# Kernel optimization log

Measured on AMD Instinct MI355X. Metric: run time of the kernel, lower is better.

Reference implementation:

```python
import jax, jax.numpy as jnp
import numpy as np

B, S, H, NH = 4, 2048, 2048, 16
HD = H // NH
EPS = 1e-5


def setup_inputs() -> dict:
    key = jax.random.key(0)
    ks = jax.random.split(key, 5)
    return {
        "x": jax.random.normal(ks[0], (B, S, H), dtype=jnp.float32),
        "ln_w": jnp.ones((H,), dtype=jnp.float32),
        "ln_b": jnp.zeros((H,), dtype=jnp.float32),
        "c_attn_w": jax.random.normal(ks[1], (H, 3 * H), dtype=jnp.float32) * 0.02,
        "c_attn_b": jax.random.normal(ks[2], (3 * H,), dtype=jnp.float32) * 0.02,
        "c_proj_w": jax.random.normal(ks[3], (H, H), dtype=jnp.float32) * 0.02,
        "c_proj_b": jax.random.normal(ks[4], (H,), dtype=jnp.float32) * 0.02,
    }


def reference(x, ln_w, ln_b, c_attn_w, c_attn_b, c_proj_w, c_proj_b):
    residual = x
    # fused layer norm
    mu = jnp.mean(x, axis=-1, keepdims=True)
    var = jnp.mean(jnp.square(x - mu), axis=-1, keepdims=True)
    xn = (x - mu) * jax.lax.rsqrt(var + EPS) * ln_w + ln_b
    qkv = jnp.einsum("bsh,hk->bsk", xn, c_attn_w) + c_attn_b
    q, k, v = jnp.split(qkv, 3, axis=-1)
    def heads(t):
        return t.reshape(B, S, NH, HD).transpose(0, 2, 1, 3)
    q, k, v = heads(q), heads(k), heads(v)
    # causal flash attention (reference math)
    scale = 1.0 / np.sqrt(HD)
    scores = jnp.einsum("bnqd,bnkd->bnqk", q, k) * scale
    causal = jnp.tril(jnp.ones((S, S), dtype=bool))
    scores = jnp.where(causal, scores, jnp.finfo(scores.dtype).min)
    attn = jax.nn.softmax(scores, axis=-1)
    o = jnp.einsum("bnqk,bnkd->bnqd", attn, v)
    # merge heads: [B,NH,S,HD] -> [B,S,H]
    o = o.transpose(0, 2, 1, 3).reshape(B, S, H)
    # output projection + residual (fused_ffn, add_gelu=False, dropout=0)
    return jnp.einsum("bsh,hk->bsk", o, c_proj_w) + c_proj_b + residual
```

## Files before the change

kernel.cpp:

```cpp
#include <hip/hip_runtime.h>
#include <stdint.h>
#include <math.h>

#define B_  4
#define S_  2048
#define H_  2048
#define NH_ 16
#define HD_ 128
#define M_  (B_*S_)
#define N3_ (3*H_)
#define NQT_ (S_/64)
#define NT_ (H_/64)

typedef __attribute__((ext_vector_type(8))) short short8;
typedef __attribute__((ext_vector_type(4))) float floatx4;
typedef unsigned int u32;

__device__ __forceinline__ unsigned short f2bf(float f) {
  unsigned u = __float_as_uint(f);
  u += 0x7FFF + ((u >> 16) & 1);
  return (unsigned short)(u >> 16);
}

__device__ __forceinline__ void gl2lds16(const void* g, void* l) {
  __builtin_amdgcn_global_load_lds(
      (const __attribute__((address_space(1))) u32*)g,
      (__attribute__((address_space(3))) u32*)l, 16, 0, 0);
}

__global__ __launch_bounds__(256) void ln_kernel(
    const float* __restrict__ x, const float* __restrict__ w,
    const float* __restrict__ b, unsigned short* __restrict__ xn) {
  int row = blockIdx.x;
  int t = threadIdx.x;
  const float* xr = x + (size_t)row * H_;
  float4 v0 = *(const float4*)(xr + t * 4);
  float4 v1 = *(const float4*)(xr + 1024 + t * 4);
  float s  = v0.x + v0.y + v0.z + v0.w + v1.x + v1.y + v1.z + v1.w;
  float sq = v0.x*v0.x + v0.y*v0.y + v0.z*v0.z + v0.w*v0.w
           + v1.x*v1.x + v1.y*v1.y + v1.z*v1.z + v1.w*v1.w;
  #pragma unroll
  for (int m = 32; m; m >>= 1) { s += __shfl_xor(s, m); sq += __shfl_xor(sq, m); }
  __shared__ float red[8];
  int wv = t >> 6;
  if ((t & 63) == 0) { red[wv * 2] = s; red[wv * 2 + 1] = sq; }
  __syncthreads();
  s  = red[0] + red[2] + red[4] + red[6];
  sq = red[1] + red[3] + red[5] + red[7];
  float mu  = s * (1.0f / H_);
  float var = sq * (1.0f / H_) - mu * mu;
  float rs  = rsqrtf(var + 1e-5f);

  float4 w0 = *(const float4*)(w + t * 4);
  float4 b0 = *(const float4*)(b + t * 4);
  float4 w1 = *(const float4*)(w + 1024 + t * 4);
  float4 b1 = *(const float4*)(b + 1024 + t * 4);
  ushort4 o0, o1;
  o0.x = f2bf((v0.x - mu) * rs * w0.x + b0.x);
  o0.y = f2bf((v0.y - mu) * rs * w0.y + b0.y);
  o0.z = f2bf((v0.z - mu) * rs * w0.z + b0.z);
  o0.w = f2bf((v0.w - mu) * rs * w0.w + b0.w);
  o1.x = f2bf((v1.x - mu) * rs * w1.x + b1.x);
  o1.y = f2bf((v1.y - mu) * rs * w1.y + b1.y);
  o1.z = f2bf((v1.z - mu) * rs * w1.z + b1.z);
  o1.w = f2bf((v1.w - mu) * rs * w1.w + b1.w);
  unsigned short* orow = xn + (size_t)row * H_;
  *(ushort4*)(orow + t * 4) = o0;
  *(ushort4*)(orow + 1024 + t * 4) = o1;
}

__global__ __launch_bounds__(256) void transpose_f2b(
    const float* __restrict__ in, unsigned short* __restrict__ out,
    int R, int C) {
  __shared__ float tile[32][33];
  int tx = threadIdx.x & 31, ty = threadIdx.x >> 5;
  int c0 = blockIdx.x * 32, r0 = blockIdx.y * 32;
  #pragma unroll
  for (int i = 0; i < 32; i += 8)
    tile[ty + i][tx] = in[(size_t)(r0 + ty + i) * C + c0 + tx];
  __syncthreads();
  #pragma unroll
  for (int i = 0; i < 32; i += 8)
    out[(size_t)(c0 + ty + i) * R + r0 + tx] = f2bf(tile[tx][ty + i]);
}

__device__ __forceinline__ void gemm256_acc(
    const unsigned short* __restrict__ A, const unsigned short* __restrict__ Bt,
    int m0, int n0, unsigned short (*sh)[16384], floatx4 (&acc)[8][4]) {
  const int t = threadIdx.x;
  const int lane = t & 63, wv = t >> 6;
  const int l15 = lane & 15, quad = lane >> 4;
  const int wm = wv >> 2, wn = wv & 3;
  const int x7 = l15 & 7;

  const int aRB = (wm * 128 + l15) * 64;
  const int bRB = (wn * 64 + l15) * 64;
  const int kx0 = ((0 + quad) ^ x7) * 8;
  const int kx1 = ((4 + quad) ^ x7) * 8;

  const int r = t >> 3, cc = t & 7;
  const int scol = (cc ^ (r & 7)) * 8;
  const unsigned short* aSrc = A + (size_t)(m0 + r) * H_ + scol;
  const int btr = (r >> 5) * 64 + (r & 31);
  const unsigned short* bSrc = Bt + (size_t)(n0 + btr) * H_ + scol;
  const int aDst = t * 8;
  const int bDst = (r >> 5) * 4096 + (r & 31) * 64 + cc * 8;

  auto stageA = [&](int kt, int reg, int buf) {
    const unsigned short* s = aSrc + (size_t)(reg * 64) * H_ + kt * 64;
    unsigned short* d = sh[buf * 2] + aDst + reg * 4096;
    gl2lds16(s, d);
    gl2lds16(s + (size_t)128 * H_, d + 8192);
  };
  auto stageB = [&](int kt, int reg, int buf) {
    const unsigned short* s = bSrc + (size_t)(reg * 32) * H_ + kt * 64;
    unsigned short* d = sh[buf * 2 + 1] + bDst + reg * 2048;
    gl2lds16(s, d);
    gl2lds16(s + (size_t)128 * H_, d + 8192);
  };

  #pragma unroll
  for (int i = 0; i < 8; i++)
    #pragma unroll
    for (int j = 0; j < 4; j++) acc[i][j] = (floatx4){0.f, 0.f, 0.f, 0.f};

  stageA(0, 0, 0); stageB(0, 0, 0); stageA(0, 1, 0); stageB(0, 1, 0);
  stageA(1, 0, 1); stageB(1, 0, 1); stageA(1, 1, 1);
  asm volatile("s_waitcnt vmcnt(6)" ::: "memory");
  __builtin_amdgcn_s_barrier();

  short8 aR[4][2], b01[2][2], b23[2][2];

  for (int n = 0; n < NT_; ++n) {
    const int buf = n & 1;
    const unsigned short* Ab = sh[buf * 2];
    const unsigned short* Bb = sh[buf * 2 + 1];

    #pragma unroll
    for (int i = 0; i < 4; ++i) {
      aR[i][0] = *(const short8*)(Ab + aRB + i * 1024 + kx0);
      aR[i][1] = *(const short8*)(Ab + aRB + i * 1024 + kx1);
    }
    #pragma unroll
    for (int j = 0; j < 2; ++j) {
      b01[j][0] = *(const short8*)(Bb + bRB + j * 1024 + kx0);
      b01[j][1] = *(const short8*)(Bb + bRB + j * 1024 + kx1);
    }
    if (n + 1 < NT_) stageB(n + 1, 1, buf ^ 1);
    asm volatile("s_waitcnt lgkmcnt(8)" ::: "memory");
    __builtin_amdgcn_s_barrier();
    asm volatile("s_waitcnt lgkmcnt(0)" ::: "memory");
    __builtin_amdgcn_sched_barrier(0);
    __builtin_amdgcn_s_setprio(1);
    #pragma unroll
    for (int i = 0; i < 4; ++i)
      #pragma unroll
      for (int j = 0; j < 2; ++j) {
        acc[i][j] = __builtin_amdgcn_mfma_f32_16x16x32_bf16(aR[i][0], b01[j][0], acc[i][j], 0, 0, 0);
        acc[i][j] = __builtin_amdgcn_mfma_f32_16x16x32_bf16(aR[i][1], b01[j][1], acc[i][j], 0, 0, 0);
      }
    __builtin_amdgcn_s_setprio(0);
    __builtin_amdgcn_s_barrier();

    #pragma unroll
    for (int j = 0; j < 2; ++j) {
      b23[j][0] = *(const short8*)(Bb + bRB + (j + 2) * 1024 + kx0);
      b23[j][1] = *(const short8*)(Bb + bRB + (j + 2) * 1024 + kx1);
    }
    if (n + 2 < NT_) stageA(n + 2, 0, buf);
    __builtin_amdgcn_s_barrier();
    asm volatile("s_waitcnt lgkmcnt(0)" ::: "memory");
    __builtin_amdgcn_sched_barrier(0);
    __builtin_amdgcn_s_setprio(1);
    #pragma unroll
    for (int i = 0; i < 4; ++i)
      #pragma unroll
      for (int j = 0; j < 2; ++j) {
        acc[i][j + 2] = __builtin_amdgcn_mfma_f32_16x16x32_bf16(aR[i][0], b23[j][0], acc[i][j + 2], 0, 0, 0);
        acc[i][j + 2] = __builtin_amdgcn_mfma_f32_16x16x32_bf16(aR[i][1], b23[j][1], acc[i][j + 2], 0, 0, 0);
      }
    __builtin_amdgcn_s_setprio(0);
    __builtin_amdgcn_s_barrier();

    #pragma unroll
    for (int i = 0; i < 4; ++i) {
      aR[i][0] = *(const short8*)(Ab + aRB + (i + 4) * 1024 + kx0);
      aR[i][1] = *(const short8*)(Ab + aRB + (i + 4) * 1024 + kx1);
    }
    if (n + 2 < NT_) stageB(n + 2, 0, buf);
    __builtin_amdgcn_s_barrier();
    asm volatile("s_waitcnt lgkmcnt(0)" ::: "memory");
    __builtin_amdgcn_sched_barrier(0);
    __builtin_amdgcn_s_setprio(1);
    #pragma unroll
    for (int i = 0; i < 4; ++i)
      #pragma unroll
      for (int j = 0; j < 2; ++j) {
        acc[i + 4][j] = __builtin_amdgcn_mfma_f32_16x16x32_bf16(aR[i][0], b01[j][0], acc[i + 4][j], 0, 0, 0);
        acc[i + 4][j] = __builtin_amdgcn_mfma_f32_16x16x32_bf16(aR[i][1], b01[j][1], acc[i + 4][j], 0, 0, 0);
      }
    __builtin_amdgcn_s_setprio(0);
    __builtin_amdgcn_s_barrier();

    if (n + 2 < NT_) stageA(n + 2, 1, buf);
    __builtin_amdgcn_s_barrier();
    __builtin_amdgcn_s_setprio(1);
    #pragma unroll
    for (int i = 0; i < 4; ++i)
      #pragma unroll
      for (int j = 0; j < 2; ++j) {
        acc[i + 4][j + 2] = __builtin_amdgcn_mfma_f32_16x16x32_bf16(aR[i][0], b23[j][0], acc[i + 4][j + 2], 0, 0, 0);
        acc[i + 4][j + 2] = __builtin_amdgcn_mfma_f32_16x16x32_bf16(aR[i][1], b23[j][1], acc[i + 4][j + 2], 0, 0, 0);
      }
    __builtin_amdgcn_s_setprio(0);
    if (n + 2 < NT_) asm volatile("s_waitcnt vmcnt(6)" ::: "memory");
    else             asm volatile("s_waitcnt vmcnt(0)" ::: "memory");
    __builtin_amdgcn_s_barrier();
  }
}

__global__ __launch_bounds__(512, 2) void qkv_gemm(
    const unsigned short* __restrict__ A, const unsigned short* __restrict__ Bt,
    const float* __restrict__ bias,
    unsigned short* __restrict__ qw, unsigned short* __restrict__ kw,
    unsigned short* __restrict__ vtw) {
  __shared__ unsigned short sh[4][16384];
  int nwg = gridDim.x * gridDim.y;
  int bid = blockIdx.y * gridDim.x + blockIdx.x;
  int swz = (bid & 7) * (nwg >> 3) + (bid >> 3);
  int n0 = (swz % gridDim.x) * 256;
  int m0 = (swz / gridDim.x) * 256;

  floatx4 acc[8][4];
  gemm256_acc(A, Bt, m0, n0, sh, acc);

  int t = threadIdx.x, lane = t & 63, wv = t >> 6;
  int l15 = lane & 15, quad = lane >> 4;
  int wm = wv >> 2, wn = wv & 3;
  int sec = n0 >> 11;
  #pragma unroll
  for (int j = 0; j < 4; ++j) {
    int nn = n0 + wn * 64 + j * 16 + l15;
    int h = (nn >> 7) & 15;
    int d = nn & 127;
    float bval = bias[nn];
    #pragma unroll
    for (int i = 0; i < 8; ++i) {
      int m = m0 + wm * 128 + i * 16 + quad * 4;
      int bb = m >> 11, s = m & 2047;
      int bh = bb * NH_ + h;
      if (sec == 2) {
        ushort4 pv;
        pv.x = f2bf(acc[i][j][0] + bval); pv.y = f2bf(acc[i][j][1] + bval);
        pv.z = f2bf(acc[i][j][2] + bval); pv.w = f2bf(acc[i][j][3] + bval);
        *(ushort4*)(vtw + ((size_t)bh * HD_ + d) * S_ + s) = pv;
      } else {
        unsigned short* dst = (sec == 0 ? qw : kw) + ((size_t)bh * S_ + s) * HD_ + d;
        #pragma unroll
        for (int reg = 0; reg < 4; reg++)
          dst[(size_t)reg * HD_] = f2bf(acc[i][j][reg] + bval);
      }
    }
  }
}

__global__ __launch_bounds__(512, 2) void proj_gemm(
    const unsigned short* __restrict__ A, const unsigned short* __restrict__ Bt,
    const float* __restrict__ bias, const float* __restrict__ resid,
    float* __restrict__ out) {
  __shared__ unsigned short sh[4][16384];
  int nwg = gridDim.x * gridDim.y;
  int bid = blockIdx.y * gridDim.x + blockIdx.x;
  int swz = (bid & 7) * (nwg >> 3) + (bid >> 3);
  int n0 = (swz % gridDim.x) * 256;
  int m0 = (swz / gridDim.x) * 256;

  floatx4 acc[8][4];
  gemm256_acc(A, Bt, m0, n0, sh, acc);

  int t = threadIdx.x, lane = t & 63, wv = t >> 6;
  int l15 = lane & 15, quad = lane >> 4;
  int wm = wv >> 2, wn = wv & 3;
  #pragma unroll
  for (int j = 0; j < 4; ++j) {
    int nn = n0 + wn * 64 + j * 16 + l15;
    float bval = bias[nn];
    #pragma unroll
    for (int i = 0; i < 8; ++i) {
      int m = m0 + wm * 128 + i * 16 + quad * 4;
      #pragma unroll
      for (int reg = 0; reg < 4; ++reg)
        out[(size_t)(m + reg) * H_ + nn] =
            acc[i][j][reg] + bval + resid[(size_t)(m + reg) * H_ + nn];
    }
  }
}

__global__ __launch_bounds__(256) void attn_kernel(
    const unsigned short* __restrict__ qw, const unsigned short* __restrict__ kw,
    const unsigned short* __restrict__ vtw, unsigned short* __restrict__ ow) {
  __shared__ unsigned short Klds[64 * 136];
  __shared__ unsigned short Vtl[128 * 72];
  __shared__ unsigned short Pl[4][16 * 72];
  int pr = blockIdx.x, bh = blockIdx.y;
  int t = threadIdx.x, lane = t & 63, wv = t >> 6;
  int l15 = lane & 15, quad = lane >> 4;
  int h = bh & 15, bb = bh >> 4;

  const float scale = 0.08838834764831845f;
  int krr = t >> 4, kcc = (t & 15) * 8;
  int vdd = t >> 3, vss = (t & 7) * 8;
  unsigned short* plw = &Pl[wv][0];
  const unsigned short* kgb = kw + ((size_t)bh * S_ + krr) * HD_ + kcc;
  const unsigned short* vgb = vtw + ((size_t)bh * HD_ + vdd) * S_ + vss;

  short8 kreg[4], vreg[4];
  auto load_stage = [&](int kb) {
    #pragma unroll
    for (int c = 0; c < 4; c++) {
      kreg[c] = *(const short8*)(kgb + (size_t)(kb + c * 16) * HD_);
      vreg[c] = *(const short8*)(vgb + (size_t)(c * 32) * S_ + kb);
    }
  };

  #pragma unroll 1
  for (int half = 0; half < 2; half++) {
    int qt = half ? (NQT_ - 1 - pr) : pr;
    int qr = qt * 64 + wv * 16;
    int q = qr + l15;

    short8 qf[4];
    {
      const unsigned short* qbase = qw + ((size_t)bh * S_ + q) * HD_ + quad * 8;
      #pragma unroll
      for (int ks = 0; ks < 4; ks++)
        qf[ks] = *(const short8*)(qbase + ks * 32);
    }

    float m_i = -INFINITY, l_i = 0.f;
    floatx4 o[8];
    #pragma unroll
    for (int ht = 0; ht < 8; ht++) o[ht] = (floatx4){0.f, 0.f, 0.f, 0.f};

    load_stage(0);
    #pragma unroll 1
    for (int kt = 0; kt <= qt; kt++) {
      int kb = kt * 64;
      __syncthreads();
      #pragma unroll
      for (int c = 0; c < 4; c++) {
        *(short8*)(Klds + (c * 16 + krr) * 136 + kcc) = kreg[c];
        *(short8*)(Vtl + (c * 32 + vdd) * 72 + vss) = vreg[c];
      }
      __syncthreads();
      if (kt < qt) load_stage(kb + 64);

      floatx4 sv[4];
      #pragma unroll
      for (int jm = 0; jm < 4; jm++) {
        sv[jm] = (floatx4){0.f, 0.f, 0.f, 0.f};
        #pragma unroll
        for (int ks = 0; ks < 4; ks++) {
          short8 kf = *(const short8*)(Klds + (jm * 16 + l15) * 136 + ks * 32 + quad * 8);
          sv[jm] = __builtin_amdgcn_mfma_f32_16x16x32_bf16(kf, qf[ks], sv[jm], 0, 0, 0);
        }
      }

      float p[4][4];
      float mx = m_i;
      #pragma unroll
      for (int jm = 0; jm < 4; jm++)
        #pragma unroll
        for (int reg = 0; reg < 4; reg++) {
          float v = sv[jm][reg] * scale;
          int key = kb + jm * 16 + quad * 4 + reg;
          if (key > q) v = -1e30f;
          p[jm][reg] = v;
          mx = fmaxf(mx, v);
        }
      mx = fmaxf(mx, __shfl_xor(mx, 16));
      mx = fmaxf(mx, __shfl_xor(mx, 32));
      float sum = 0.f;
      #pragma unroll
      for (int jm = 0; jm < 4; jm++)
        #pragma unroll
        for (int reg = 0; reg < 4; reg++) { p[jm][reg] = __expf(p[jm][reg] - mx); sum += p[jm][reg]; }
      sum += __shfl_xor(sum, 16);
      sum += __shfl_xor(sum, 32);
      float alpha = __expf(m_i - mx);
      l_i = l_i * alpha + sum;
      m_i = mx;
      #pragma unroll
      for (int ht = 0; ht < 8; ht++) o[ht] *= alpha;

      #pragma unroll
      for (int jm = 0; jm < 4; jm++) {
        ushort4 pk;
        pk.x = f2bf(p[jm][0]); pk.y = f2bf(p[jm][1]);
        pk.z = f2bf(p[jm][2]); pk.w = f2bf(p[jm][3]);
        *(ushort4*)(plw + l15 * 72 + jm * 16 + quad * 4) = pk;
      }

      #pragma unroll
      for (int ks2 = 0; ks2 < 2; ks2++) {
        short8 pf = *(const short8*)(plw + l15 * 72 + ks2 * 32 + quad * 8);
        #pragma unroll
        for (int ht = 0; ht < 8; ht++) {
          short8 vf = *(const short8*)(Vtl + (ht * 16 + l15) * 72 + ks2 * 32 + quad * 8);
          o[ht] = __builtin_amdgcn_mfma_f32_16x16x32_bf16(vf, pf, o[ht], 0, 0, 0);
        }
      }
    }

    float inv = 1.0f / l_i;
    size_t base = ((size_t)(bb * S_ + q)) * H_ + h * HD_ + quad * 4;
    #pragma unroll
    for (int ht = 0; ht < 8; ht++) {
      ushort4 ov;
      ov.x = f2bf(o[ht][0] * inv); ov.y = f2bf(o[ht][1] * inv);
      ov.z = f2bf(o[ht][2] * inv); ov.w = f2bf(o[ht][3] * inv);
      *(ushort4*)(ow + base + ht * 16) = ov;
    }
  }
}

extern "C" void kernel_launch(void* const* d_in, const int* in_sizes, int n_in,
                              void* d_out, int out_size, void* d_ws, size_t ws_size,
                              hipStream_t stream) {
  (void)in_sizes; (void)n_in; (void)out_size; (void)ws_size;
  const float* x      = (const float*)d_in[0];
  const float* ln_w   = (const float*)d_in[1];
  const float* ln_b   = (const float*)d_in[2];
  const float* attn_w = (const float*)d_in[3];
  const float* attn_b = (const float*)d_in[4];
  const float* proj_w = (const float*)d_in[5];
  const float* proj_b = (const float*)d_in[6];
  float* out = (float*)d_out;

  char* ws = (char*)d_ws;
  size_t off = 0;
  auto alloc = [&](size_t bytes) {
    char* p = ws + off;
    off += (bytes + 255) & ~(size_t)255;
    return p;
  };
  unsigned short* xn     = (unsigned short*)alloc((size_t)M_ * H_ * 2);
  unsigned short* wqkvt  = (unsigned short*)alloc((size_t)N3_ * H_ * 2);
  unsigned short* wprojt = (unsigned short*)alloc((size_t)H_ * H_ * 2);
  unsigned short* qws    = (unsigned short*)alloc((size_t)M_ * H_ * 2);
  unsigned short* kws    = (unsigned short*)alloc((size_t)M_ * H_ * 2);
  unsigned short* vtws   = (unsigned short*)alloc((size_t)M_ * H_ * 2);
  unsigned short* attn_out = xn;

  ln_kernel<<<M_, 256, 0, stream>>>(x, ln_w, ln_b, xn);
  transpose_f2b<<<dim3(N3_ / 32, H_ / 32), 256, 0, stream>>>(attn_w, wqkvt, H_, N3_);
  transpose_f2b<<<dim3(H_ / 32, H_ / 32), 256, 0, stream>>>(proj_w, wprojt, H_, H_);
  qkv_gemm<<<dim3(N3_ / 256, M_ / 256), 512, 0, stream>>>(xn, wqkvt, attn_b, qws, kws, vtws);
  attn_kernel<<<dim3(NQT_ / 2, B_ * NH_), 256, 0, stream>>>(qws, kws, vtws, attn_out);
  proj_gemm<<<dim3(H_ / 256, M_ / 256), 512, 0, stream>>>(attn_out, wprojt, proj_b, x, out);
}
```

Before: 619.0 us.

## Remap GEMM tiles per XCD, lazy softmax rescale, MFMA priority in attention

Replaces the GEMM block swizzle with an XCD-aware mapping that gives each XCD a contiguous group of four M-tiles, aiming to improve L2 reuse of A tiles. In the attention kernel, the online-softmax rescale of the output accumulators is skipped unless some lane's new max exceeds the running max by more than 8, saving the per-tile multiply of o. It also raises wave priority around the QK and PV MFMA blocks. The lazy rescale lets exp values grow up to e^8 before renormalising, which stays safe in fp32 but changes rounding slightly. The new tile mapping assumes a particular grid shape, 32 M-tiles and a block count divisible by 8.

```diff
diff --git a/kernel.cpp b/kernel.cpp
--- a/kernel.cpp
+++ b/kernel.cpp
@@ -219,17 +219,21 @@
   }
 }
 
+__device__ __forceinline__ void xcd_map(int& m0, int& n0) {
+  int bid = blockIdx.y * gridDim.x + blockIdx.x;
+  int xcd = bid & 7, loc = bid >> 3;
+  m0 = ((xcd << 2) | (loc & 3)) * 256;
+  n0 = (loc >> 2) * 256;
+}
+
 __global__ __launch_bounds__(512, 2) void qkv_gemm(
     const unsigned short* __restrict__ A, const unsigned short* __restrict__ Bt,
     const float* __restrict__ bias,
     unsigned short* __restrict__ qw, unsigned short* __restrict__ kw,
     unsigned short* __restrict__ vtw) {
   __shared__ unsigned short sh[4][16384];
-  int nwg = gridDim.x * gridDim.y;
-  int bid = blockIdx.y * gridDim.x + blockIdx.x;
-  int swz = (bid & 7) * (nwg >> 3) + (bid >> 3);
-  int n0 = (swz % gridDim.x) * 256;
-  int m0 = (swz / gridDim.x) * 256;
+  int m0, n0;
+  xcd_map(m0, n0);
 
   floatx4 acc[8][4];
   gemm256_acc(A, Bt, m0, n0, sh, acc);
@@ -269,11 +273,8 @@
     const float* __restrict__ bias, const float* __restrict__ resid,
     float* __restrict__ out) {
   __shared__ unsigned short sh[4][16384];
-  int nwg = gridDim.x * gridDim.y;
-  int bid = blockIdx.y * gridDim.x + blockIdx.x;
-  int swz = (bid & 7) * (nwg >> 3) + (bid >> 3);
-  int n0 = (swz % gridDim.x) * 256;
-  int m0 = (swz / gridDim.x) * 256;
+  int m0, n0;
+  xcd_map(m0, n0);
 
   floatx4 acc[8][4];
   gemm256_acc(A, Bt, m0, n0, sh, acc);
@@ -356,6 +357,7 @@
       if (kt < qt) load_stage(kb + 64);
 
       floatx4 sv[4];
+      __builtin_amdgcn_s_setprio(1);
       #pragma unroll
       for (int jm = 0; jm < 4; jm++) {
         sv[jm] = (floatx4){0.f, 0.f, 0.f, 0.f};
@@ -365,9 +367,10 @@
           sv[jm] = __builtin_amdgcn_mfma_f32_16x16x32_bf16(kf, qf[ks], sv[jm], 0, 0, 0);
         }
       }
+      __builtin_amdgcn_s_setprio(0);
 
       float p[4][4];
-      float mx = m_i;
+      float pmax = -INFINITY;
       #pragma unroll
       for (int jm = 0; jm < 4; jm++)
         #pragma unroll
@@ -376,22 +379,26 @@
           int key = kb + jm * 16 + quad * 4 + reg;
           if (key > q) v = -1e30f;
           p[jm][reg] = v;
-          mx = fmaxf(mx, v);
+          pmax = fmaxf(pmax, v);
         }
-      mx = fmaxf(mx, __shfl_xor(mx, 16));
-      mx = fmaxf(mx, __shfl_xor(mx, 32));
+      pmax = fmaxf(pmax, __shfl_xor(pmax, 16));
+      pmax = fmaxf(pmax, __shfl_xor(pmax, 32));
+      if (!__all(pmax - m_i <= 8.f)) {
+        float mnew = fmaxf(m_i, pmax);
+        float alpha = __expf(m_i - mnew);
+        l_i *= alpha;
+        #pragma unroll
+        for (int ht = 0; ht < 8; ht++) o[ht] *= alpha;
+        m_i = mnew;
+      }
       float sum = 0.f;
       #pragma unroll
       for (int jm = 0; jm < 4; jm++)
         #pragma unroll
-        for (int reg = 0; reg < 4; reg++) { p[jm][reg] = __expf(p[jm][reg] - mx); sum += p[jm][reg]; }
+        for (int reg = 0; reg < 4; reg++) { p[jm][reg] = __expf(p[jm][reg] - m_i); sum += p[jm][reg]; }
       sum += __shfl_xor(sum, 16);
       sum += __shfl_xor(sum, 32);
-      float alpha = __expf(m_i - mx);
-      l_i = l_i * alpha + sum;
-      m_i = mx;
-      #pragma unroll
-      for (int ht = 0; ht < 8; ht++) o[ht] *= alpha;
+      l_i += sum;
 
       #pragma unroll
       for (int jm = 0; jm < 4; jm++) {
@@ -401,6 +408,7 @@
         *(ushort4*)(plw + l15 * 72 + jm * 16 + quad * 4) = pk;
       }
 
+      __builtin_amdgcn_s_setprio(1);
       #pragma unroll
       for (int ks2 = 0; ks2 < 2; ks2++) {
         short8 pf = *(const short8*)(plw + l15 * 72 + ks2 * 32 + quad * 8);
@@ -410,6 +418,7 @@
           o[ht] = __builtin_amdgcn_mfma_f32_16x16x32_bf16(vf, pf, o[ht], 0, 0, 0);
         }
       }
+      __builtin_amdgcn_s_setprio(0);
     }
 
     float inv = 1.0f / l_i;
```

Result: no change. 625.2 us (+1.0%).
